# Kernel tuning notes

Measured on AMD Instinct MI355X. Metric: run time of the kernel, lower is better.

## Reference

```python
import jax, jax.numpy as jnp
import numpy as np

B, N, CIN, COUT, R, K = 8, 4096, 64, 128, 32, 3
GROUPS = 8
GN_EPS = 1e-5


def setup_inputs() -> dict:
    key = jax.random.key(0)
    ks = jax.random.split(key, 6)
    w = lambda k, shape, fan: jax.random.normal(k, shape, jnp.float32) / np.sqrt(fan)
    return dict(
        features=jax.random.normal(ks[0], (B, CIN, N), jnp.float32),
        coords=jax.random.uniform(ks[1], (B, N, 3), jnp.float32),
        conv1_w=w(ks[2], (COUT, CIN, K, K, K), CIN * K ** 3), conv1_b=jnp.zeros((COUT,), jnp.float32),
        gn1_g=jnp.ones((COUT,), jnp.float32), gn1_b=jnp.zeros((COUT,), jnp.float32),
        conv2_w=w(ks[3], (COUT, COUT, K, K, K), COUT * K ** 3), conv2_b=jnp.zeros((COUT,), jnp.float32),
        gn2_g=jnp.ones((COUT,), jnp.float32), gn2_b=jnp.zeros((COUT,), jnp.float32),
        pt_w=w(ks[4], (COUT, CIN), CIN), pt_b=jnp.zeros((COUT,), jnp.float32),
        ptgn_g=jnp.ones((COUT,), jnp.float32), ptgn_b=jnp.zeros((COUT,), jnp.float32),
    )


def swish(x):
    return x * jax.nn.sigmoid(x)


def group_norm(x, gamma, beta):
    # x: [B, C, *spatial]
    b, c = x.shape[0], x.shape[1]
    sp = x.shape[2:]
    xg = x.reshape(b, GROUPS, -1)
    m = xg.mean(-1, keepdims=True)
    v = xg.var(-1, keepdims=True)
    xg = (xg - m) * jax.lax.rsqrt(v + GN_EPS)
    x = xg.reshape(b, c, *sp)
    shape = (1, c) + (1,) * len(sp)
    return x * gamma.reshape(shape) + beta.reshape(shape)


def conv3d(x, w, bias):
    p = K // 2
    y = jax.lax.conv_general_dilated(
        x, w, window_strides=(1, 1, 1), padding=[(p, p)] * 3,
        dimension_numbers=('NCDHW', 'OIDHW', 'NCDHW'))
    return y + bias[None, :, None, None, None]


def voxelize(features, coords):
    # PVCNN avg_voxelize: normalize coords to [0, R-1], round, scatter-mean.
    c = coords - coords.mean(axis=1, keepdims=True)          # [B,N,3]
    scale = 2.0 * jnp.linalg.norm(c, axis=-1).max(axis=1)     # [B], eps=0
    norm_coords = c / scale[:, None, None] + 0.5
    norm_coords = jnp.clip(norm_coords * R, 0.0, R - 1)       # float coords in [0, R-1]
    vox = jnp.round(norm_coords).astype(jnp.int32)
    flat = (vox[..., 0] * R + vox[..., 1]) * R + vox[..., 2]  # [B,N]
    seg = (flat + jnp.arange(B, dtype=jnp.int32)[:, None] * R ** 3).reshape(-1)
    ft = features.transpose(0, 2, 1).reshape(B * N, CIN)
    sums = jax.ops.segment_sum(ft, seg, num_segments=B * R ** 3)
    cnt = jax.ops.segment_sum(jnp.ones((B * N,), ft.dtype), seg, num_segments=B * R ** 3)
    grid = sums / jnp.maximum(cnt, 1.0)[:, None]
    grid = grid.reshape(B, R ** 3, CIN).transpose(0, 2, 1).reshape(B, CIN, R, R, R)
    return grid, norm_coords


def trilinear_devoxelize(grid, norm_coords):
    # grid: [B, C, R, R, R]; norm_coords: [B, N, 3] float in [0, R-1]
    c = grid.shape[1]
    f = jnp.floor(norm_coords)
    d = norm_coords - f                                       # frac, [B,N,3]
    f0 = f.astype(jnp.int32)
    f1 = jnp.minimum(f0 + 1, R - 1)
    gridf = grid.reshape(B, c, R ** 3)
    out = jnp.zeros((B, c, N), grid.dtype)
    for ix in (0, 1):
        for iy in (0, 1):
            for iz in (0, 1):
                xi = f1[..., 0] if ix else f0[..., 0]
                yi = f1[..., 1] if iy else f0[..., 1]
                zi = f1[..., 2] if iz else f0[..., 2]
                wx = d[..., 0] if ix else 1.0 - d[..., 0]
                wy = d[..., 1] if iy else 1.0 - d[..., 1]
                wz = d[..., 2] if iz else 1.0 - d[..., 2]
                idx = (xi * R + yi) * R + zi                  # [B,N]
                g = jnp.take_along_axis(gridf, idx[:, None, :], axis=2)  # [B,C,N]
                out = out + g * (wx * wy * wz)[:, None, :]
    return out


def reference(features, coords, conv1_w, conv1_b, gn1_g, gn1_b,
              conv2_w, conv2_b, gn2_g, gn2_b, pt_w, pt_b, ptgn_g, ptgn_b):
    grid, norm_coords = voxelize(features, coords)
    h = swish(group_norm(conv3d(grid, conv1_w, conv1_b), gn1_g, gn1_b))
    h = swish(group_norm(conv3d(h, conv2_w, conv2_b), gn2_g, gn2_b))
    devox = trilinear_devoxelize(h, norm_coords)              # [B, COUT, N]
    pf = jnp.einsum('oc,bcn->bon', pt_w, features) + pt_b[None, :, None]
    pf = swish(group_norm(pf, ptgn_g, ptgn_b))
    return devox + pf
```

## Files before the change

### kernel.cpp

```cpp
#include <hip/hip_runtime.h>
#include <hip/hip_bf16.h>
#include <cstdint>

#define B_ 8
#define N_ 4096
#define CIN_ 64
#define COUT_ 128
#define R_ 32
#define R3_ 32768
#define GROUPS_ 8
#define EPS_ 1e-5f

typedef float f32x4 __attribute__((ext_vector_type(4)));
typedef __bf16 bf16x8 __attribute__((ext_vector_type(8)));
typedef unsigned short ushort8x __attribute__((ext_vector_type(8)));

static __device__ __forceinline__ unsigned short f2b(float f) {
    uint32_t u = __float_as_uint(f);
    uint32_t r = (u + 0x7fffu + ((u >> 16) & 1u)) >> 16;
    return (unsigned short)r;
}
static __device__ __forceinline__ float b2f(unsigned short u) {
    return __uint_as_float(((uint32_t)u) << 16);
}
static __device__ __forceinline__ float fswish(float s) {
    return s * __builtin_amdgcn_rcpf(1.0f + __expf(-s));
}

__global__ void k_batch_stats(const float* __restrict__ coords, float* __restrict__ bstats) {
    int b = blockIdx.x;
    int tid = threadIdx.x;
    __shared__ float rb[256];
    __shared__ float smean[3];
    const float* cb = coords + (size_t)b * N_ * 3;
    float sx = 0.f, sy = 0.f, sz = 0.f;
    for (int n = tid; n < N_; n += 256) {
        sx += cb[n * 3 + 0];
        sy += cb[n * 3 + 1];
        sz += cb[n * 3 + 2];
    }
    float vals[3] = {sx, sy, sz};
    for (int k = 0; k < 3; ++k) {
        rb[tid] = vals[k];
        __syncthreads();
        for (int s = 128; s > 0; s >>= 1) {
            if (tid < s) rb[tid] += rb[tid + s];
            __syncthreads();
        }
        if (tid == 0) smean[k] = rb[0] / (float)N_;
        __syncthreads();
    }
    float mx = smean[0], my = smean[1], mz = smean[2];
    float m2 = 0.f;
    for (int n = tid; n < N_; n += 256) {
        float dx = cb[n * 3 + 0] - mx, dy = cb[n * 3 + 1] - my, dz = cb[n * 3 + 2] - mz;
        m2 = fmaxf(m2, dx * dx + dy * dy + dz * dz);
    }
    rb[tid] = m2;
    __syncthreads();
    for (int s = 128; s > 0; s >>= 1) {
        if (tid < s) rb[tid] = fmaxf(rb[tid], rb[tid + s]);
        __syncthreads();
    }
    if (tid == 0) {
        bstats[b * 4 + 0] = mx;
        bstats[b * 4 + 1] = my;
        bstats[b * 4 + 2] = mz;
        bstats[b * 4 + 3] = 2.0f * sqrtf(rb[0]);
    }
}

__global__ void k_points(const float* __restrict__ coords, const float* __restrict__ bstats,
                         float* __restrict__ ncoords, int* __restrict__ flatidx,
                         float* __restrict__ cnt) {
    int idx = blockIdx.x * 256 + threadIdx.x;
    int b = idx >> 12, n = idx & (N_ - 1);
    float scale = bstats[b * 4 + 3];
    int vi[3];
    for (int k = 0; k < 3; ++k) {
        float c = coords[((size_t)b * N_ + n) * 3 + k] - bstats[b * 4 + k];
        float nc = fminf(fmaxf((c / scale + 0.5f) * (float)R_, 0.0f), (float)(R_ - 1));
        ncoords[((size_t)b * N_ + n) * 3 + k] = nc;
        vi[k] = (int)rintf(nc);
    }
    int flat = (vi[0] * R_ + vi[1]) * R_ + vi[2];
    flatidx[idx] = flat;
    atomicAdd(&cnt[(size_t)b * R3_ + flat], 1.0f);
}

__global__ void k_scatter(const float* __restrict__ feat, const int* __restrict__ flatidx,
                          float* __restrict__ vox, int b0) {
    int bid = blockIdx.x;
    int nch = bid & 15, ci = (bid >> 4) & 63, bl = bid >> 10;
    int b = b0 + bl;
    int n = nch * 256 + threadIdx.x;
    float v = feat[((size_t)b * CIN_ + ci) * N_ + n];
    int flat = flatidx[b * N_ + n];
    atomicAdd(&vox[((size_t)bl * R3_ + flat) * CIN_ + ci], v);
}

__global__ void k_divide(const float* __restrict__ vox, const float* __restrict__ cnt,
                         unsigned short* __restrict__ gA, int b0) {
    size_t idx8 = (size_t)blockIdx.x * 256 + threadIdx.x;
    size_t voxel = idx8 >> 3;
    float c = cnt[(size_t)b0 * R3_ + voxel];
    float s = 1.0f / fmaxf(c, 1.0f);
    const float4* v4 = (const float4*)vox;
    float4 a = v4[idx8 * 2], b = v4[idx8 * 2 + 1];
    ushort8x o;
    o[0] = f2b(a.x * s); o[1] = f2b(a.y * s); o[2] = f2b(a.z * s); o[3] = f2b(a.w * s);
    o[4] = f2b(b.x * s); o[5] = f2b(b.y * s); o[6] = f2b(b.z * s); o[7] = f2b(b.w * s);
    ((ushort8x*)gA)[idx8] = o;
}

__global__ void k_feat2b(const float* __restrict__ f, unsigned short* __restrict__ fb, int b0) {
    size_t i8 = (size_t)blockIdx.x * 256 + threadIdx.x;
    const float4* s = (const float4*)(f + (size_t)b0 * CIN_ * N_);
    float4 a = s[i8 * 2], b = s[i8 * 2 + 1];
    ushort8x o;
    o[0] = f2b(a.x); o[1] = f2b(a.y); o[2] = f2b(a.z); o[3] = f2b(a.w);
    o[4] = f2b(b.x); o[5] = f2b(b.y); o[6] = f2b(b.z); o[7] = f2b(b.w);
    ((ushort8x*)fb)[i8] = o;
}

__global__ void k_wpack16(const float* __restrict__ w, unsigned short* __restrict__ wp,
                          int Cin, int taps) {
    int e = blockIdx.x * 256 + threadIdx.x;
    int total = taps * Cin * 128;
    if (e >= total) return;
    int KC = Cin / 32;
    int j = e & 7;
    int l = (e >> 3) & 63;
    int rest = e >> 9;
    int ct = rest & 7;
    int stepk = rest >> 3;
    int kc = stepk % KC;
    int t = stepk / KC;
    int co = ct * 16 + (l & 15);
    int ci = kc * 32 + (l >> 4) * 8 + j;
    wp[e] = f2b(w[((size_t)co * Cin + ci) * taps + t]);
}

__global__ void k_gnswish(unsigned short* __restrict__ g, const float* __restrict__ stats,
                          const float* __restrict__ gamma, const float* __restrict__ beta,
                          int b0) {
    size_t idx8 = (size_t)blockIdx.x * 256 + threadIdx.x;
    int c0 = (int)(idx8 & 15) * 8;
    int b = b0 + (int)(idx8 >> 19);
    int grp = c0 >> 4;
    const float cntv = 16.0f * R3_;
    float mean = stats[(b * 8 + grp) * 2 + 0] / cntv;
    float var = stats[(b * 8 + grp) * 2 + 1] / cntv - mean * mean;
    float inv = rsqrtf(var + EPS_);
    ushort8x v = ((ushort8x*)g)[idx8];
#pragma unroll
    for (int k = 0; k < 8; ++k) {
        float A = gamma[c0 + k] * inv;
        float Bc = beta[c0 + k] - mean * A;
        v[k] = f2b(fswish(A * b2f(v[k]) + Bc));
    }
    ((ushort8x*)g)[idx8] = v;
}

template <int CIN>
__global__ __launch_bounds__(128, 2) void k_conv16(
    const unsigned short* __restrict__ in, const unsigned short* __restrict__ wp,
    const float* __restrict__ bias, unsigned short* __restrict__ out,
    float* __restrict__ stats, int b0) {
    constexpr int KC = CIN / 32;
    constexpr int S = CIN + 8;
    __shared__ unsigned short abuf[6 * 34 * S];
    __shared__ float s_sum[8], s_sq[8];
    int tid = threadIdx.x;
    int bid = blockIdx.x;
    int yg = bid & 7, x = (bid >> 3) & 31, bl = bid >> 8;
    int y0 = yg * 4;
    int lane = tid & 63, zt = tid >> 6;
    int mrow = lane & 15, quad = lane >> 4;

    if (tid < 8) { s_sum[tid] = 0.f; s_sq[tid] = 0.f; }
    for (int i = tid; i < 6 * 2 * (CIN / 8); i += 128) {
        int cy = i / (2 * (CIN / 8));
        int r = i - cy * (2 * (CIN / 8));
        int hz = (r >= (CIN / 8)) ? 33 : 0;
        int c8 = r % (CIN / 8);
        ushort8x zz = {0, 0, 0, 0, 0, 0, 0, 0};
        *(ushort8x*)&abuf[(cy * 34 + hz) * S + c8 * 8] = zz;
    }

    float bv[8];
#pragma unroll
    for (int ct = 0; ct < 8; ++ct) bv[ct] = bias[ct * 16 + mrow];
    f32x4 acc[4][8];
#pragma unroll
    for (int yc = 0; yc < 4; ++yc)
#pragma unroll
        for (int ct = 0; ct < 8; ++ct) {
            acc[yc][ct][0] = bv[ct]; acc[yc][ct][1] = bv[ct];
            acc[yc][ct][2] = bv[ct]; acc[yc][ct][3] = bv[ct];
        }

    for (int xxi = 0; xxi < 3; ++xxi) {
        int xx = x + xxi - 1;
        if (xx < 0 || xx >= 32) continue;
        __syncthreads();
        for (int i = tid; i < 6 * 32 * (CIN / 8); i += 128) {
            int cy = i / (32 * (CIN / 8));
            int r = i - cy * (32 * (CIN / 8));
            int z = r / (CIN / 8), c8 = r - z * (CIN / 8);
            int yy = y0 - 1 + cy;
            ushort8x v = {0, 0, 0, 0, 0, 0, 0, 0};
            if (yy >= 0 && yy < 32)
                v = *(const ushort8x*)&in[((size_t)bl * R3_ + xx * 1024 + yy * 32 + z) * CIN + c8 * 8];
            *(ushort8x*)&abuf[(cy * 34 + z + 1) * S + c8 * 8] = v;
        }
        __syncthreads();

        for (int dy3 = 0; dy3 < 3; ++dy3) {
            for (int dz = 0; dz < 3; ++dz) {
                int t = (xxi * 3 + dy3) * 3 + dz;
#pragma unroll
                for (int kc = 0; kc < KC; ++kc) {
                    const unsigned short* wbase =
                        wp + ((size_t)((t * KC + kc) * 8) * 64 + lane) * 8;
                    bf16x8 bfr[8];
#pragma unroll
                    for (int ct = 0; ct < 8; ++ct)
                        bfr[ct] = *(const bf16x8*)(wbase + ct * 512);
#pragma unroll
                    for (int yc = 0; yc < 4; ++yc) {
                        int cy = yc + dy3;
                        bf16x8 a = *(const bf16x8*)
                            &abuf[(cy * 34 + zt * 16 + mrow + dz) * S + kc * 32 + quad * 8];
#pragma unroll
                        for (int ct = 0; ct < 8; ++ct)
                            acc[yc][ct] = __builtin_amdgcn_mfma_f32_16x16x32_bf16(
                                a, bfr[ct], acc[yc][ct], 0, 0, 0);
                    }
                }
            }
        }
    }

    float lsum[8] = {0.f, 0.f, 0.f, 0.f, 0.f, 0.f, 0.f, 0.f};
    float lsq[8] = {0.f, 0.f, 0.f, 0.f, 0.f, 0.f, 0.f, 0.f};
#pragma unroll
    for (int yc = 0; yc < 4; ++yc) {
        int y = y0 + yc;
        unsigned short* obase = out + ((size_t)bl * R3_ + x * 1024 + y * 32) * 128;
#pragma unroll
        for (int ct = 0; ct < 8; ++ct) {
            int co = ct * 16 + mrow;
#pragma unroll
            for (int r = 0; r < 4; ++r) {
                int z = zt * 16 + quad * 4 + r;
                float vv = acc[yc][ct][r];
                obase[(size_t)z * 128 + co] = f2b(vv);
                lsum[ct] += vv;
                lsq[ct] += vv * vv;
            }
        }
    }
#pragma unroll
    for (int ct = 0; ct < 8; ++ct) {
        float s = lsum[ct], q = lsq[ct];
#pragma unroll
        for (int off = 32; off >= 1; off >>= 1) {
            s += __shfl_xor(s, off);
            q += __shfl_xor(q, off);
        }
        if (lane == 0) {
            atomicAdd(&s_sum[ct], s);
            atomicAdd(&s_sq[ct], q);
        }
    }
    __syncthreads();
    if (tid < 8) {
        int b = b0 + bl;
        atomicAdd(&stats[((size_t)b * 8 + tid) * 2 + 0], s_sum[tid]);
        atomicAdd(&stats[((size_t)b * 8 + tid) * 2 + 1], s_sq[tid]);
    }
}

__global__ __launch_bounds__(256) void k_point_mfma(
    const unsigned short* __restrict__ featb, const unsigned short* __restrict__ wp,
    const float* __restrict__ bias, unsigned short* __restrict__ pf,
    float* __restrict__ stats, int b0) {
    __shared__ __align__(16) unsigned short ALds[256 * 72];
    int tid = threadIdx.x;
    int bid = blockIdx.x;
    int bl = bid >> 4;
    int n0 = (bid & 15) * 256;
    int b = b0 + bl;
    int lane = tid & 63, wv = tid >> 6;
    int nh = wv & 1, ch = wv >> 1;
    int mrow = lane & 15, quad = lane >> 4;

    {
        int c0 = (tid >> 5) * 8;
        int nl = tid & 31;
        for (int u = 0; u < 8; ++u) {
            int n = u * 32 + nl;
            ushort8x v;
#pragma unroll
            for (int k = 0; k < 8; ++k)
                v[k] = featb[((size_t)(bl * 64 + c0 + k)) * N_ + n0 + n];
            *(ushort8x*)&ALds[n * 72 + c0] = v;
        }
    }

    bf16x8 bfr[2][4];
#pragma unroll
    for (int kc = 0; kc < 2; ++kc)
#pragma unroll
        for (int ct = 0; ct < 4; ++ct)
            bfr[kc][ct] = *(const bf16x8*)&wp[((size_t)((kc * 8) + ch * 4 + ct) * 64 + lane) * 8];

    float bv[4];
#pragma unroll
    for (int ct = 0; ct < 4; ++ct) bv[ct] = bias[ch * 64 + ct * 16 + mrow];
    f32x4 acc[8][4];
#pragma unroll
    for (int mt = 0; mt < 8; ++mt)
#pragma unroll
        for (int ct = 0; ct < 4; ++ct) {
            acc[mt][ct][0] = bv[ct]; acc[mt][ct][1] = bv[ct];
            acc[mt][ct][2] = bv[ct]; acc[mt][ct][3] = bv[ct];
        }

    __syncthreads();
#pragma unroll
    for (int kc = 0; kc < 2; ++kc) {
#pragma unroll
        for (int mt = 0; mt < 8; ++mt) {
            bf16x8 a = *(const bf16x8*)
                &ALds[(nh * 128 + mt * 16 + mrow) * 72 + kc * 32 + quad * 8];
#pragma unroll
            for (int ct = 0; ct < 4; ++ct)
                acc[mt][ct] = __builtin_amdgcn_mfma_f32_16x16x32_bf16(
                    a, bfr[kc][ct], acc[mt][ct], 0, 0, 0);
        }
    }

#pragma unroll
    for (int ct = 0; ct < 4; ++ct) {
        int co = ch * 64 + ct * 16 + mrow;
        float s = 0.f, q = 0.f;
#pragma unroll
        for (int mt = 0; mt < 8; ++mt) {
#pragma unroll
            for (int r = 0; r < 4; ++r) {
                int n = nh * 128 + mt * 16 + quad * 4 + r;
                float vv = acc[mt][ct][r];
                pf[((size_t)bl * N_ + n0 + n) * 128 + co] = f2b(vv);
                s += vv;
                q += vv * vv;
            }
        }
#pragma unroll
        for (int off = 32; off >= 1; off >>= 1) {
            s += __shfl_xor(s, off);
            q += __shfl_xor(q, off);
        }
        if (lane == 0) {
            int g = ch * 4 + ct;
            atomicAdd(&stats[((size_t)b * 8 + g) * 2 + 0], s);
            atomicAdd(&stats[((size_t)b * 8 + g) * 2 + 1], q);
        }
    }
}

__global__ __launch_bounds__(256) void k_final(
    const unsigned short* __restrict__ grid, const float* __restrict__ ncoords,
    const unsigned short* __restrict__ pf,
    const float* __restrict__ stats2, const float* __restrict__ g2g,
    const float* __restrict__ g2b,
    const float* __restrict__ statsPt, const float* __restrict__ pgg,
    const float* __restrict__ pgb,
    float* __restrict__ out, int b0) {
    __shared__ int sidx[32][8];
    __shared__ float swt[32][8];
    __shared__ float devt[32 * 129];
    int bid = blockIdx.x;
    int bl = bid >> 7;
    int b = b0 + bl;
    int n0 = (bid & 127) * 32;
    int tid = threadIdx.x;
    if (tid < 32) {
        int n = n0 + tid;
        const float* nc = ncoords + ((size_t)b * N_ + n) * 3;
        float fc[3] = {nc[0], nc[1], nc[2]};
        int i0[3], i1[3];
        float dd[3];
        for (int k = 0; k < 3; ++k) {
            float fl = floorf(fc[k]);
            i0[k] = (int)fl;
            i1[k] = min(i0[k] + 1, R_ - 1);
            dd[k] = fc[k] - fl;
        }
#pragma unroll
        for (int k = 0; k < 8; ++k) {
            int ix = (k >> 2) & 1, iy = (k >> 1) & 1, iz = k & 1;
            int xi = ix ? i1[0] : i0[0];
            int yi = iy ? i1[1] : i0[1];
            int zi = iz ? i1[2] : i0[2];
            sidx[tid][k] = (xi * R_ + yi) * R_ + zi;
            float wx = ix ? dd[0] : 1.0f - dd[0];
            float wy = iy ? dd[1] : 1.0f - dd[1];
            float wz = iz ? dd[2] : 1.0f - dd[2];
            swt[tid][k] = wx * wy * wz;
        }
    }
    __syncthreads();
    int co = tid & 127, pg = tid >> 7;
    int grp = co >> 4;
    const float ic2 = 1.0f / (16.0f * R3_);
    float mean2 = stats2[(b * 8 + grp) * 2 + 0] * ic2;
    float var2 = stats2[(b * 8 + grp) * 2 + 1] * ic2 - mean2 * mean2;
    float inv2 = rsqrtf(var2 + EPS_);
    float A2 = g2g[co] * inv2, B2 = g2b[co] - mean2 * A2;
    const float icp = 1.0f / (16.0f * N_);
    float meanp = statsPt[(b * 8 + grp) * 2 + 0] * icp;
    float varp = statsPt[(b * 8 + grp) * 2 + 1] * icp - meanp * meanp;
    float invp = rsqrtf(varp + EPS_);
    float Ap = pgg[co] * invp, Bp = pgb[co] - meanp * Ap;

    const unsigned short* gp = grid + (size_t)bl * R3_ * 128 + co;
    for (int p = pg; p < 32; p += 2) {
        float acc = 0.f;
#pragma unroll
        for (int k = 0; k < 8; ++k) {
            float s = A2 * b2f(gp[(size_t)sidx[p][k] * 128]) + B2;
            acc += swt[p][k] * fswish(s);
        }
        float xv = b2f(pf[((size_t)bl * N_ + n0 + p) * 128 + co]);
        devt[p * 129 + co] = acc + fswish(Ap * xv + Bp);
    }
    __syncthreads();
    int pp = tid & 31, cg = tid >> 5;
    float* op = out + (size_t)b * 128 * N_ + n0 + pp;
    for (int c = cg * 16; c < cg * 16 + 16; ++c)
        op[(size_t)c * N_] = devt[pp * 129 + c];
}

extern "C" void kernel_launch(void* const* d_in, const int* in_sizes, int n_in,
                              void* d_out, int out_size, void* d_ws, size_t ws_size,
                              hipStream_t stream) {
    const float* features = (const float*)d_in[0];
    const float* coords = (const float*)d_in[1];
    const float* c1w = (const float*)d_in[2];
    const float* c1b = (const float*)d_in[3];
    const float* g1g = (const float*)d_in[4];
    const float* g1b = (const float*)d_in[5];
    const float* c2w = (const float*)d_in[6];
    const float* c2b = (const float*)d_in[7];
    const float* g2g = (const float*)d_in[8];
    const float* g2b = (const float*)d_in[9];
    const float* ptw = (const float*)d_in[10];
    const float* ptb = (const float*)d_in[11];
    const float* pgg = (const float*)d_in[12];
    const float* pgb = (const float*)d_in[13];
    float* outp = (float*)d_out;

    size_t globals = ((size_t)B_ * R3_ * 4 + 255 & ~(size_t)255)
                   + ((size_t)B_ * N_ * 3 * 4 + 255 & ~(size_t)255)
                   + ((size_t)B_ * N_ * 4 + 255 & ~(size_t)255)
                   + 256 + 2048
                   + ((size_t)27 * 64 * 128 * 2 + 255 & ~(size_t)255)
                   + ((size_t)27 * 128 * 128 * 2 + 255 & ~(size_t)255)
                   + ((size_t)64 * 128 * 2 + 255 & ~(size_t)255)
                   + 8192;
    int CB = 1;
    for (int cb = 8; cb >= 1; cb >>= 1) {
        size_t need = globals
                    + ((size_t)cb * R3_ * 64 * 4)
                    + ((size_t)cb * R3_ * 64 * 2)
                    + ((size_t)cb * R3_ * 128 * 2)
                    + ((size_t)cb * N_ * 128 * 2)
                    + ((size_t)cb * 64 * N_ * 2);
        if (need <= ws_size) { CB = cb; break; }
    }

    char* ws = (char*)d_ws;
    size_t o = 0;
    auto alloc = [&](size_t bytes) {
        size_t r = o;
        o += (bytes + 255) & ~(size_t)255;
        return r;
    };
    float* voxC = (float*)(ws + alloc((size_t)CB * R3_ * 64 * 4));
    unsigned short* gC = (unsigned short*)voxC;
    unsigned short* gA = (unsigned short*)(ws + alloc((size_t)CB * R3_ * 64 * 2));
    unsigned short* gB = (unsigned short*)(ws + alloc((size_t)CB * R3_ * 128 * 2));
    unsigned short* pfbuf = (unsigned short*)(ws + alloc((size_t)CB * N_ * 128 * 2));
    unsigned short* featbc = (unsigned short*)(ws + alloc((size_t)CB * 64 * N_ * 2));
    float* cnt = (float*)(ws + alloc((size_t)B_ * R3_ * 4));
    float* ncoords = (float*)(ws + alloc((size_t)B_ * N_ * 3 * 4));
    int* flatidx = (int*)(ws + alloc((size_t)B_ * N_ * 4));
    float* bstats = (float*)(ws + alloc(256));
    float* statsAll = (float*)(ws + alloc(2048));
    float* stats1 = statsAll;
    float* stats2 = statsAll + 128;
    float* statsPt = statsAll + 256;
    unsigned short* wp1 = (unsigned short*)(ws + alloc((size_t)27 * 64 * 128 * 2));
    unsigned short* wp2 = (unsigned short*)(ws + alloc((size_t)27 * 128 * 128 * 2));
    unsigned short* wpPt = (unsigned short*)(ws + alloc((size_t)64 * 128 * 2));

    hipMemsetAsync(cnt, 0, (size_t)B_ * R3_ * 4, stream);
    hipMemsetAsync(statsAll, 0, 1536, stream);
    k_wpack16<<<(27 * 64 * 128 + 255) / 256, 256, 0, stream>>>(c1w, wp1, 64, 27);
    k_wpack16<<<(27 * 128 * 128 + 255) / 256, 256, 0, stream>>>(c2w, wp2, 128, 27);
    k_wpack16<<<(64 * 128 + 255) / 256, 256, 0, stream>>>(ptw, wpPt, 64, 1);
    k_batch_stats<<<B_, 256, 0, stream>>>(coords, bstats);
    k_points<<<B_ * N_ / 256, 256, 0, stream>>>(coords, bstats, ncoords, flatidx, cnt);

    for (int b0 = 0; b0 < B_; b0 += CB) {
        hipMemsetAsync(voxC, 0, (size_t)CB * R3_ * 64 * 4, stream);
        k_feat2b<<<CB * 128, 256, 0, stream>>>(features, featbc, b0);
        k_scatter<<<CB * 64 * 16, 256, 0, stream>>>(features, flatidx, voxC, b0);
        k_divide<<<CB * 1024, 256, 0, stream>>>(voxC, cnt, gA, b0);
        k_conv16<64><<<CB * 256, 128, 0, stream>>>(gA, wp1, c1b, gB, stats1, b0);
        k_gnswish<<<CB * 2048, 256, 0, stream>>>(gB, stats1, g1g, g1b, b0);
        k_conv16<128><<<CB * 256, 128, 0, stream>>>(gB, wp2, c2b, gC, stats2, b0);
        k_point_mfma<<<CB * 16, 256, 0, stream>>>(featbc, wpPt, ptb, pfbuf, statsPt, b0);
        k_final<<<CB * 128, 256, 0, stream>>>(gC, ncoords, pfbuf,
                                              stats2, g2g, g2b, statsPt, pgg, pgb, outp, b0);
    }
}
```

Measured before the change: 763.1 us.

## Split conv work across four waves by y-pair and output-channel half

The 3D conv kernel moves from 128 threads (2 waves, each covering 16 z by 4 y by 128 channels) to 256 threads (4 waves, each covering 2 y by 32 z by 64 channels). Each wave now needs fewer accumulators and loads only half the weight fragments. The z-halo padding rows in shared memory are replaced by one shared zero row selected by a bounds check, which shrinks LDS use. The batch-stats kernel also goes to 1024 threads. The cost is a per-load branch or select for the z boundary, and the loss of the explicit two-blocks-per-SM occupancy hint.

New measurement: 617.3 us. 19.1% less time.

```diff
diff --git a/kernel.cpp b/kernel.cpp
--- a/kernel.cpp
+++ b/kernel.cpp
@@ -30,11 +30,11 @@
 __global__ void k_batch_stats(const float* __restrict__ coords, float* __restrict__ bstats) {
     int b = blockIdx.x;
     int tid = threadIdx.x;
-    __shared__ float rb[256];
+    __shared__ float rb[1024];
     __shared__ float smean[3];
     const float* cb = coords + (size_t)b * N_ * 3;
     float sx = 0.f, sy = 0.f, sz = 0.f;
-    for (int n = tid; n < N_; n += 256) {
+    for (int n = tid; n < N_; n += 1024) {
         sx += cb[n * 3 + 0];
         sy += cb[n * 3 + 1];
         sz += cb[n * 3 + 2];
@@ -43,7 +43,7 @@
     for (int k = 0; k < 3; ++k) {
         rb[tid] = vals[k];
         __syncthreads();
-        for (int s = 128; s > 0; s >>= 1) {
+        for (int s = 512; s > 0; s >>= 1) {
             if (tid < s) rb[tid] += rb[tid + s];
             __syncthreads();
         }
@@ -52,13 +52,13 @@
     }
     float mx = smean[0], my = smean[1], mz = smean[2];
     float m2 = 0.f;
-    for (int n = tid; n < N_; n += 256) {
+    for (int n = tid; n < N_; n += 1024) {
         float dx = cb[n * 3 + 0] - mx, dy = cb[n * 3 + 1] - my, dz = cb[n * 3 + 2] - mz;
         m2 = fmaxf(m2, dx * dx + dy * dy + dz * dz);
     }
     rb[tid] = m2;
     __syncthreads();
-    for (int s = 128; s > 0; s >>= 1) {
+    for (int s = 512; s > 0; s >>= 1) {
         if (tid < s) rb[tid] = fmaxf(rb[tid], rb[tid + s]);
         __syncthreads();
     }
@@ -163,48 +163,48 @@
 }
 
 template <int CIN>
-__global__ __launch_bounds__(128, 2) void k_conv16(
+__global__ __launch_bounds__(256) void k_conv(
     const unsigned short* __restrict__ in, const unsigned short* __restrict__ wp,
     const float* __restrict__ bias, unsigned short* __restrict__ out,
     float* __restrict__ stats, int b0) {
     constexpr int KC = CIN / 32;
     constexpr int S = CIN + 8;
-    __shared__ unsigned short abuf[6 * 34 * S];
+    constexpr int ZP = 6 * 32 * S;
+    __shared__ __align__(16) unsigned short abuf[(6 * 32 + 1) * S];
     __shared__ float s_sum[8], s_sq[8];
     int tid = threadIdx.x;
     int bid = blockIdx.x;
     int yg = bid & 7, x = (bid >> 3) & 31, bl = bid >> 8;
     int y0 = yg * 4;
-    int lane = tid & 63, zt = tid >> 6;
+    int lane = tid & 63, wv = tid >> 6;
+    int yp = wv & 1, ch = wv >> 1;
     int mrow = lane & 15, quad = lane >> 4;
 
     if (tid < 8) { s_sum[tid] = 0.f; s_sq[tid] = 0.f; }
-    for (int i = tid; i < 6 * 2 * (CIN / 8); i += 128) {
-        int cy = i / (2 * (CIN / 8));
-        int r = i - cy * (2 * (CIN / 8));
-        int hz = (r >= (CIN / 8)) ? 33 : 0;
-        int c8 = r % (CIN / 8);
+    for (int i = tid; i < S / 8; i += 256) {
         ushort8x zz = {0, 0, 0, 0, 0, 0, 0, 0};
-        *(ushort8x*)&abuf[(cy * 34 + hz) * S + c8 * 8] = zz;
-    }
-
-    float bv[8];
-#pragma unroll
-    for (int ct = 0; ct < 8; ++ct) bv[ct] = bias[ct * 16 + mrow];
-    f32x4 acc[4][8];
-#pragma unroll
-    for (int yc = 0; yc < 4; ++yc)
-#pragma unroll
-        for (int ct = 0; ct < 8; ++ct) {
-            acc[yc][ct][0] = bv[ct]; acc[yc][ct][1] = bv[ct];
-            acc[yc][ct][2] = bv[ct]; acc[yc][ct][3] = bv[ct];
-        }
+        *(ushort8x*)&abuf[ZP + i * 8] = zz;
+    }
+
+    float bv[4];
+#pragma unroll
+    for (int ct = 0; ct < 4; ++ct) bv[ct] = bias[ch * 64 + ct * 16 + mrow];
+    f32x4 acc[2][2][4];
+#pragma unroll
+    for (int a = 0; a < 2; ++a)
+#pragma unroll
+        for (int zt = 0; zt < 2; ++zt)
+#pragma unroll
+            for (int ct = 0; ct < 4; ++ct) {
+                acc[a][zt][ct][0] = bv[ct]; acc[a][zt][ct][1] = bv[ct];
+                acc[a][zt][ct][2] = bv[ct]; acc[a][zt][ct][3] = bv[ct];
+            }
 
     for (int xxi = 0; xxi < 3; ++xxi) {
         int xx = x + xxi - 1;
         if (xx < 0 || xx >= 32) continue;
         __syncthreads();
-        for (int i = tid; i < 6 * 32 * (CIN / 8); i += 128) {
+        for (int i = tid; i < 6 * 32 * (CIN / 8); i += 256) {
             int cy = i / (32 * (CIN / 8));
             int r = i - cy * (32 * (CIN / 8));
             int z = r / (CIN / 8), c8 = r - z * (CIN / 8);
@@ -212,7 +212,7 @@
             ushort8x v = {0, 0, 0, 0, 0, 0, 0, 0};
             if (yy >= 0 && yy < 32)
                 v = *(const ushort8x*)&in[((size_t)bl * R3_ + xx * 1024 + yy * 32 + z) * CIN + c8 * 8];
-            *(ushort8x*)&abuf[(cy * 34 + z + 1) * S + c8 * 8] = v;
+            *(ushort8x*)&abuf[(cy * 32 + z) * S + c8 * 8] = v;
         }
         __syncthreads();
 
@@ -222,47 +222,55 @@
 #pragma unroll
                 for (int kc = 0; kc < KC; ++kc) {
                     const unsigned short* wbase =
-                        wp + ((size_t)((t * KC + kc) * 8) * 64 + lane) * 8;
-                    bf16x8 bfr[8];
-#pragma unroll
-                    for (int ct = 0; ct < 8; ++ct)
+                        wp + ((size_t)((t * KC + kc) * 8 + ch * 4) * 64 + lane) * 8;
+                    bf16x8 bfr[4];
+#pragma unroll
+                    for (int ct = 0; ct < 4; ++ct)
                         bfr[ct] = *(const bf16x8*)(wbase + ct * 512);
 #pragma unroll
-                    for (int yc = 0; yc < 4; ++yc) {
-                        int cy = yc + dy3;
-                        bf16x8 a = *(const bf16x8*)
-                            &abuf[(cy * 34 + zt * 16 + mrow + dz) * S + kc * 32 + quad * 8];
-#pragma unroll
-                        for (int ct = 0; ct < 8; ++ct)
-                            acc[yc][ct] = __builtin_amdgcn_mfma_f32_16x16x32_bf16(
-                                a, bfr[ct], acc[yc][ct], 0, 0, 0);
+                    for (int yo2 = 0; yo2 < 2; ++yo2) {
+                        int cy = yp * 2 + yo2 + dy3;
+#pragma unroll
+                        for (int zt = 0; zt < 2; ++zt) {
+                            int z = zt * 16 + mrow + dz - 1;
+                            int off = (z >= 0 && z < 32)
+                                          ? (cy * 32 + z) * S + kc * 32 + quad * 8
+                                          : ZP + kc * 32 + quad * 8;
+                            bf16x8 a = *(const bf16x8*)&abuf[off];
+#pragma unroll
+                            for (int ct = 0; ct < 4; ++ct)
+                                acc[yo2][zt][ct] = __builtin_amdgcn_mfma_f32_16x16x32_bf16(
+                                    a, bfr[ct], acc[yo2][zt][ct], 0, 0, 0);
+                        }
                     }
                 }
             }
         }
     }
 
-    float lsum[8] = {0.f, 0.f, 0.f, 0.f, 0.f, 0.f, 0.f, 0.f};
-    float lsq[8] = {0.f, 0.f, 0.f, 0.f, 0.f, 0.f, 0.f, 0.f};
-#pragma unroll
-    for (int yc = 0; yc < 4; ++yc) {
-        int y = y0 + yc;
+    float lsum[4] = {0.f, 0.f, 0.f, 0.f}, lsq[4] = {0.f, 0.f, 0.f, 0.f};
+#pragma unroll
+    for (int yo2 = 0; yo2 < 2; ++yo2) {
+        int y = y0 + yp * 2 + yo2;
         unsigned short* obase = out + ((size_t)bl * R3_ + x * 1024 + y * 32) * 128;
 #pragma unroll
-        for (int ct = 0; ct < 8; ++ct) {
-            int co = ct * 16 + mrow;
-#pragma unroll
-            for (int r = 0; r < 4; ++r) {
-                int z = zt * 16 + quad * 4 + r;
-                float vv = acc[yc][ct][r];
-                obase[(size_t)z * 128 + co] = f2b(vv);
-                lsum[ct] += vv;
-                lsq[ct] += vv * vv;
+        for (int zt = 0; zt < 2; ++zt) {
+#pragma unroll
+            for (int ct = 0; ct < 4; ++ct) {
+                int co = ch * 64 + ct * 16 + mrow;
+#pragma unroll
+                for (int r = 0; r < 4; ++r) {
+                    int z = zt * 16 + quad * 4 + r;
+                    float vv = acc[yo2][zt][ct][r];
+                    obase[(size_t)z * 128 + co] = f2b(vv);
+                    lsum[ct] += vv;
+                    lsq[ct] += vv * vv;
+                }
             }
         }
     }
 #pragma unroll
-    for (int ct = 0; ct < 8; ++ct) {
+    for (int ct = 0; ct < 4; ++ct) {
         float s = lsum[ct], q = lsq[ct];
 #pragma unroll
         for (int off = 32; off >= 1; off >>= 1) {
@@ -270,8 +278,8 @@
             q += __shfl_xor(q, off);
         }
         if (lane == 0) {
-            atomicAdd(&s_sum[ct], s);
-            atomicAdd(&s_sq[ct], q);
+            atomicAdd(&s_sum[ch * 4 + ct], s);
+            atomicAdd(&s_sq[ch * 4 + ct], q);
         }
     }
     __syncthreads();
@@ -511,7 +519,7 @@
     k_wpack16<<<(27 * 64 * 128 + 255) / 256, 256, 0, stream>>>(c1w, wp1, 64, 27);
     k_wpack16<<<(27 * 128 * 128 + 255) / 256, 256, 0, stream>>>(c2w, wp2, 128, 27);
     k_wpack16<<<(64 * 128 + 255) / 256, 256, 0, stream>>>(ptw, wpPt, 64, 1);
-    k_batch_stats<<<B_, 256, 0, stream>>>(coords, bstats);
+    k_batch_stats<<<B_, 1024, 0, stream>>>(coords, bstats);
     k_points<<<B_ * N_ / 256, 256, 0, stream>>>(coords, bstats, ncoords, flatidx, cnt);
 
     for (int b0 = 0; b0 < B_; b0 += CB) {
@@ -519,9 +527,9 @@
         k_feat2b<<<CB * 128, 256, 0, stream>>>(features, featbc, b0);
         k_scatter<<<CB * 64 * 16, 256, 0, stream>>>(features, flatidx, voxC, b0);
         k_divide<<<CB * 1024, 256, 0, stream>>>(voxC, cnt, gA, b0);
-        k_conv16<64><<<CB * 256, 128, 0, stream>>>(gA, wp1, c1b, gB, stats1, b0);
+        k_conv<64><<<CB * 256, 256, 0, stream>>>(gA, wp1, c1b, gB, stats1, b0);
         k_gnswish<<<CB * 2048, 256, 0, stream>>>(gB, stats1, g1g, g1b, b0);
-        k_conv16<128><<<CB * 256, 128, 0, stream>>>(gB, wp2, c2b, gC, stats2, b0);
+        k_conv<128><<<CB * 256, 256, 0, stream>>>(gB, wp2, c2b, gC, stats2, b0);
         k_point_mfma<<<CB * 16, 256, 0, stream>>>(featbc, wpPt, ptb, pfbuf, statsPt, b0);
         k_final<<<CB * 128, 256, 0, stream>>>(gC, ncoords, pfbuf,
                                               stats2, g2g, g2b, statsPt, pgg, pgb, outp, b0);
```
